# Performance work log

Measured on AMD Instinct MI355X. Metric: run time of the kernel, lower is better.

Reference implementation:

```python
import jax, jax.numpy as jnp
import numpy as np

COLB = 16            # COL_BLOCK_WIDTH
IN_W = 1024          # input_width; zero_inputs=0 so input_locations = arange(IN_W)
OUT_W = 512          # output_width
DEPTH = 8            # network_depth
IN_L = 4             # butterfly_in_depth
OUT_L = 4            # butterfly_out_depth
ACT = 8              # activations_per_block
BLOCKS = 64          # blocks_per_layer -> num_inputs = 1024 per module
CURV = 1.0
GROW = BLOCKS * ACT  # 512 new rows per module
TOTAL = IN_W + DEPTH * GROW  # 5120
BATCH = 4096


def setup_inputs() -> dict:
    key = jax.random.key(0)
    k1, k2, k3 = jax.random.split(key, 3)
    input_data = jax.random.normal(k1, (IN_W, BATCH), dtype=jnp.float32)
    scales = jnp.full((IN_W,), 0.05, dtype=jnp.float32)
    # angles uniform in (-pi, pi), shape [depth, in_layers+out_layers, num_inputs/2]
    angles = (jax.random.uniform(k2, (DEPTH, IN_L + OUT_L, BLOCKS * COLB // 2)) * 2.0 - 1.0) * np.pi
    angles = angles.astype(jnp.float32)
    biases = jax.random.normal(k3, (DEPTH, GROW), dtype=jnp.float32) * 0.05
    # per-module indices_in = randperm(total_width_so_far)[:num_inputs]
    rng = np.random.RandomState(0)
    tw = IN_W
    idxs = []
    for _ in range(DEPTH):
        idxs.append(rng.permutation(tw)[: BLOCKS * COLB].astype(np.int32))
        tw += GROW
    indices_in = jnp.asarray(np.stack(idxs))  # [depth, 1024]
    return {"input_data": input_data, "scales": scales, "angles": angles,
            "biases": biases, "indices_in": indices_in}


def _rotate(x, ang, stride):
    # x: [W, B]; pair row i (with (i//stride)%2==0) with row i+stride inside 16-blocks
    W, B = x.shape
    xr = x.reshape(W // (2 * stride), 2, stride, B)
    a = ang.reshape(W // (2 * stride), stride)[:, :, None]
    c, s = jnp.cos(a), jnp.sin(a)
    lo, hi = xr[:, 0], xr[:, 1]              # [W/2s, s, B]
    nlo = c * lo + s * hi
    nhi = -s * lo + c * hi
    return jnp.stack([nlo, nhi], axis=1).reshape(W, B)


def _butterfly_module(data, ang, bias, idx, idx_out):
    W = BLOCKS * COLB
    x = data[idx]                             # gather [1024, B]
    for l in range(IN_L):
        x = _rotate(x, ang[l], 2 ** (l % 4))
    xb = x.reshape(BLOCKS, COLB, -1)
    pre = xb[:, :ACT, :] + bias.reshape(BLOCKS, ACT)[:, :, None]
    # curvature (smoothed-ReLU) activation
    act = 0.5 * (pre + jnp.sqrt(pre * pre + CURV * CURV))
    xb = xb.at[:, :ACT, :].set(act)
    x = xb.reshape(W, -1)
    for l in range(OUT_L):
        x = _rotate(x, ang[IN_L + l], 2 ** ((IN_L + l) % 4))
    data = data.at[idx].set(x)                # scatter working set back
    data = data.at[idx_out: idx_out + GROW].set(act.reshape(GROW, -1))
    return data


def reference(input_data, scales, angles, biases, indices_in):
    B = input_data.shape[1]
    data = jnp.zeros((TOTAL, B), dtype=input_data.dtype)
    data = data.at[:IN_W].set(scales[:, None] * input_data)
    for i in range(DEPTH):
        data = _butterfly_module(data, angles[i], biases[i], indices_in[i], IN_W + GROW * i)
    return data[TOTAL - OUT_W:]
```

## Files before the change

kernel.cpp:

```cpp
#include <hip/hip_runtime.h>
#include <math.h>

#define N_INW     1024
#define N_DEPTH   8
#define N_GROW    512
#define N_BATCH   4096
#define N_THREADS 128
#define N_LAYERS  64
#define SLAB_B    19584

typedef __attribute__((ext_vector_type(2))) float    F2;
typedef __attribute__((ext_vector_type(2))) _Float16 h2;

__global__ void precompute_kernel(const float* __restrict__ angles,
                                  const int*   __restrict__ indices,
                                  _Float16* __restrict__ csh,
                                  int*   __restrict__ addrs) {
    int i = blockIdx.x * blockDim.x + threadIdx.x;
    if (i < N_LAYERS * 512) {
        int g = i >> 9, p = i & 511, blk = p >> 3, j = p & 7;
        float a = angles[i];
        _Float16* base = csh + g * 1024 + blk * 16;
        base[j]     = (_Float16)cosf(a);
        base[8 + j] = (_Float16)sinf(a);
    }
    if (i < N_DEPTH * N_INW) {
        int v = indices[i];
        addrs[i] = (v + (v >> 4)) << 2;
    }
}

#define ADDR(r) ((((r) + ((r) >> 4))) << 2)

#define LDH(A)    __builtin_bit_cast(h2, *(const unsigned*)(L + (A)))
#define STH(A, V) do { *(unsigned*)(L + (A)) =                                 \
                       __builtin_bit_cast(unsigned, (V)); } while (0)

#define PKU(x, y) __builtin_bit_cast(unsigned int,                             \
                      __builtin_amdgcn_cvt_pkrtz((x), (y)))

#define BCL(U) ({ h2 _t = __builtin_bit_cast(h2, (unsigned)(U));               \
                  h2 _r; _r.x = _t.x; _r.y = _t.x; _r; })
#define BCH(U) ({ h2 _t = __builtin_bit_cast(h2, (unsigned)(U));               \
                  h2 _r; _r.x = _t.y; _r.y = _t.y; _r; })

#define ROTPH(LO, HI, CC, SS) do { h2 _l = LO, _h = HI, _c = CC, _s = SS;      \
    LO = _c * _l + _s * _h; HI = _c * _h - _s * _l; } while (0)

#define DECL_SET(P)                                                            \
    uint4 P##c0, P##s0, P##c1, P##s1, P##c2, P##s2, P##c3, P##s3,              \
          P##c4, P##s4, P##c5, P##s5, P##c6, P##s6, P##c7, P##s7;              \
    int4  P##i0, P##i1, P##i2, P##i3;                                          \
    float4 P##bA, P##bB;

#define SYN1(P, K, ANB) do {                                                   \
    const float4* _p = (const float4*)((ANB) + (K)*512 + (blk << 3));          \
    float4 _u = _p[0], _v = _p[1];                                             \
    float _c0,_c1,_c2,_c3,_c4,_c5,_c6,_c7,_t0,_t1,_t2,_t3,_t4,_t5,_t6,_t7;     \
    __sincosf(_u.x,&_t0,&_c0); __sincosf(_u.y,&_t1,&_c1);                      \
    __sincosf(_u.z,&_t2,&_c2); __sincosf(_u.w,&_t3,&_c3);                      \
    __sincosf(_v.x,&_t4,&_c4); __sincosf(_v.y,&_t5,&_c5);                      \
    __sincosf(_v.z,&_t6,&_c6); __sincosf(_v.w,&_t7,&_c7);                      \
    P##c##K = make_uint4(PKU(_c0,_c1),PKU(_c2,_c3),PKU(_c4,_c5),PKU(_c6,_c7)); \
    P##s##K = make_uint4(PKU(_t0,_t1),PKU(_t2,_t3),PKU(_t4,_t5),PKU(_t6,_t7)); \
  } while (0)

#define LOADCS1(P, K, CSN, ANB) do { if (USE_TABLE) {                          \
    const char* _b = (CSN) + (blk << 5) + (K)*2048;                            \
    P##c##K = *(const uint4*)(_b); P##s##K = *(const uint4*)(_b + 16);         \
  } else { SYN1(P, K, ANB); } } while (0)

#define LOADCS8(P, CSN, ANB) do {                                              \
    LOADCS1(P,0,CSN,ANB); LOADCS1(P,1,CSN,ANB); LOADCS1(P,2,CSN,ANB);          \
    LOADCS1(P,3,CSN,ANB); LOADCS1(P,4,CSN,ANB); LOADCS1(P,5,CSN,ANB);          \
    LOADCS1(P,6,CSN,ANB); LOADCS1(P,7,CSN,ANB); } while (0)
#define LOADCS4(P, CSN, ANB) do {                                              \
    LOADCS1(P,0,CSN,ANB); LOADCS1(P,1,CSN,ANB); LOADCS1(P,2,CSN,ANB);          \
    LOADCS1(P,3,CSN,ANB); } while (0)

#define TR(v) (((v) + ((v) >> 4)) << 2)
#define LOAD_AB(P, ATN, INB, BIN) do { if (USE_TABLE) {                        \
    const int4* _ip = (const int4*)((ATN) + (blk << 4));                       \
    P##i0=_ip[0]; P##i1=_ip[1]; P##i2=_ip[2]; P##i3=_ip[3];                    \
  } else {                                                                     \
    const int4* _ip = (const int4*)((INB) + (blk << 4));                       \
    int4 _v0=_ip[0], _v1=_ip[1], _v2=_ip[2], _v3=_ip[3];                       \
    P##i0.x=TR(_v0.x); P##i0.y=TR(_v0.y); P##i0.z=TR(_v0.z); P##i0.w=TR(_v0.w);\
    P##i1.x=TR(_v1.x); P##i1.y=TR(_v1.y); P##i1.z=TR(_v1.z); P##i1.w=TR(_v1.w);\
    P##i2.x=TR(_v2.x); P##i2.y=TR(_v2.y); P##i2.z=TR(_v2.z); P##i2.w=TR(_v2.w);\
    P##i3.x=TR(_v3.x); P##i3.y=TR(_v3.y); P##i3.z=TR(_v3.z); P##i3.w=TR(_v3.w);\
  }                                                                            \
  const float4* _bp = (const float4*)((BIN) + (blk << 3));                     \
  P##bA = _bp[0]; P##bB = _bp[1]; } while (0)

#define HROTS1(C,S) do {                                                       \
    ROTPH(x0,x1,  BCL(C.x),BCL(S.x)); ROTPH(x2,x3,  BCH(C.x),BCH(S.x));        \
    ROTPH(x4,x5,  BCL(C.y),BCL(S.y)); ROTPH(x6,x7,  BCH(C.y),BCH(S.y));        \
    ROTPH(x8,x9,  BCL(C.z),BCL(S.z)); ROTPH(x10,x11,BCH(C.z),BCH(S.z));        \
    ROTPH(x12,x13,BCL(C.w),BCL(S.w)); ROTPH(x14,x15,BCH(C.w),BCH(S.w));        \
  } while (0)
#define HROTS2(C,S) do {                                                       \
    ROTPH(x0,x2,  BCL(C.x),BCL(S.x)); ROTPH(x1,x3,  BCH(C.x),BCH(S.x));        \
    ROTPH(x4,x6,  BCL(C.y),BCL(S.y)); ROTPH(x5,x7,  BCH(C.y),BCH(S.y));        \
    ROTPH(x8,x10, BCL(C.z),BCL(S.z)); ROTPH(x9,x11, BCH(C.z),BCH(S.z));        \
    ROTPH(x12,x14,BCL(C.w),BCL(S.w)); ROTPH(x13,x15,BCH(C.w),BCH(S.w));        \
  } while (0)
#define HROTS4(C,S) do {                                                       \
    ROTPH(x0,x4,  BCL(C.x),BCL(S.x)); ROTPH(x1,x5,  BCH(C.x),BCH(S.x));        \
    ROTPH(x2,x6,  BCL(C.y),BCL(S.y)); ROTPH(x3,x7,  BCH(C.y),BCH(S.y));        \
    ROTPH(x8,x12, BCL(C.z),BCL(S.z)); ROTPH(x9,x13, BCH(C.z),BCH(S.z));        \
    ROTPH(x10,x14,BCL(C.w),BCL(S.w)); ROTPH(x11,x15,BCH(C.w),BCH(S.w));        \
  } while (0)
#define HROTS8(C,S) do {                                                       \
    ROTPH(x0,x8,  BCL(C.x),BCL(S.x)); ROTPH(x1,x9,  BCH(C.x),BCH(S.x));        \
    ROTPH(x2,x10, BCL(C.y),BCL(S.y)); ROTPH(x3,x11, BCH(C.y),BCH(S.y));        \
    ROTPH(x4,x12, BCL(C.z),BCL(S.z)); ROTPH(x5,x13, BCH(C.z),BCH(S.z));        \
    ROTPH(x6,x14, BCL(C.w),BCL(S.w)); ROTPH(x7,x15, BCH(C.w),BCH(S.w));        \
  } while (0)

#define HROT(P, K, M) M(P##c##K, P##s##K)

#define ACTH(X, BF) do {                                                       \
    float _lo = (float)(X).x + (BF), _hi = (float)(X).y + (BF);                \
    _lo = 0.5f * (_lo + __builtin_amdgcn_sqrtf(_lo * _lo + 1.0f));             \
    _hi = 0.5f * (_hi + __builtin_amdgcn_sqrtf(_hi * _hi + 1.0f));             \
    X = __builtin_bit_cast(h2, PKU(_lo, _hi)); } while (0)

#define FENCE() __builtin_amdgcn_sched_barrier(0)

#define PROC_MOD(P, N, CSN, ANN, ATN, INB, BIN, M, FULL) do {                  \
  const int a0=P##i0.x, a1=P##i0.y, a2=P##i0.z, a3=P##i0.w,                    \
            a4=P##i1.x, a5=P##i1.y, a6=P##i1.z, a7=P##i1.w,                    \
            a8=P##i2.x, a9=P##i2.y, a10=P##i2.z, a11=P##i2.w,                  \
            a12=P##i3.x, a13=P##i3.y, a14=P##i3.z, a15=P##i3.w;                \
  h2 x0=LDH(a0), x1=LDH(a1), x2=LDH(a2), x3=LDH(a3),                           \
     x4=LDH(a4), x5=LDH(a5), x6=LDH(a6), x7=LDH(a7),                           \
     x8=LDH(a8), x9=LDH(a9), x10=LDH(a10), x11=LDH(a11),                       \
     x12=LDH(a12), x13=LDH(a13), x14=LDH(a14), x15=LDH(a15);                   \
  if (FULL) { LOADCS8(N, CSN, ANN); } else { LOADCS4(N, CSN, ANN); }           \
  FENCE();                                                                     \
  HROT(P,0,HROTS1); HROT(P,1,HROTS2); HROT(P,2,HROTS4); HROT(P,3,HROTS8);      \
  ACTH(x0,P##bA.x); ACTH(x1,P##bA.y); ACTH(x2,P##bA.z); ACTH(x3,P##bA.w);      \
  ACTH(x4,P##bB.x); ACTH(x5,P##bB.y); ACTH(x6,P##bB.z); ACTH(x7,P##bB.w);      \
  const int _ab = ADDR(N_INW + (M)*N_GROW + (blk << 3));                       \
  STH(_ab+ 0,x0); STH(_ab+ 4,x1); STH(_ab+ 8,x2); STH(_ab+12,x3);              \
  STH(_ab+16,x4); STH(_ab+20,x5); STH(_ab+24,x6); STH(_ab+28,x7);              \
  LOAD_AB(N, ATN, INB, BIN);                                                   \
  FENCE();                                                                     \
  HROT(P,4,HROTS1); HROT(P,5,HROTS2); HROT(P,6,HROTS4); HROT(P,7,HROTS8);      \
  STH(a0,x0);  STH(a1,x1);  STH(a2,x2);  STH(a3,x3);                           \
  STH(a4,x4);  STH(a5,x5);  STH(a6,x6);  STH(a7,x7);                           \
  STH(a8,x8);  STH(a9,x9);  STH(a10,x10); STH(a11,x11);                        \
  STH(a12,x12); STH(a13,x13); STH(a14,x14); STH(a15,x15);                      \
} while (0)

template <bool USE_TABLE>
__global__ __launch_bounds__(N_THREADS, 2)
void butterfly_fused_kernel(const float* __restrict__ input,
                            const float* __restrict__ scales,
                            const float* __restrict__ biases,
                            const int*   __restrict__ indices,
                            const char*  __restrict__ cs_tab,
                            const int*   __restrict__ addr_tab,
                            const float* __restrict__ angles,
                            float* __restrict__ out) {
    extern __shared__ float ldsbuf[];
    const int t   = threadIdx.x;
    const int blk = t & 63;
    const int cp  = t >> 6;
    char* L = (char*)ldsbuf + cp * SLAB_B;
    const int b   = blockIdx.x;
    const int cg  = ((((b & 7) * 128) + (b >> 3)) << 2) + (cp << 1);

    DECL_SET(A) DECL_SET(B)

    LOADCS8(A, cs_tab, angles);
    LOAD_AB(A, addr_tab, indices, biases);

#pragma unroll
    for (int k = 0; k < 16; ++k) {
        const int r = (k << 6) + blk;
        F2 v = *(const F2*)(input + (size_t)r * N_BATCH + cg);
        STH(ADDR(r), __builtin_bit_cast(h2, PKU(scales[r] * v.x, scales[r] * v.y)));
    }

    const char*  csn = cs_tab + 16384;
    const float* ann = angles + 4096;
    const int*   atn = addr_tab + N_INW;
    const int*   inb = indices + N_INW;
    const float* bin = biases + N_GROW;

#pragma unroll 1
    for (int tt = 0; tt < 3; ++tt) {
        const int m = 2 * tt;
        PROC_MOD(A, B, csn, ann, atn, inb, bin, m, 1);
        csn += 16384; ann += 4096; atn += N_INW; inb += N_INW; bin += N_GROW;
        PROC_MOD(B, A, csn, ann, atn, inb, bin, m + 1, 1);
        csn += 16384; ann += 4096; atn += N_INW; inb += N_INW; bin += N_GROW;
    }
    PROC_MOD(A, B, csn, ann, atn, inb, bin, 6, 0);

    {
        h2 x0=LDH(Bi0.x), x1=LDH(Bi0.y), x2=LDH(Bi0.z), x3=LDH(Bi0.w),
           x4=LDH(Bi1.x), x5=LDH(Bi1.y), x6=LDH(Bi1.z), x7=LDH(Bi1.w),
           x8=LDH(Bi2.x), x9=LDH(Bi2.y), x10=LDH(Bi2.z), x11=LDH(Bi2.w),
           x12=LDH(Bi3.x), x13=LDH(Bi3.y), x14=LDH(Bi3.z), x15=LDH(Bi3.w);
        FENCE();
        HROT(B,0,HROTS1); HROT(B,1,HROTS2); HROT(B,2,HROTS4); HROT(B,3,HROTS8);
        ACTH(x0,BbA.x); ACTH(x1,BbA.y); ACTH(x2,BbA.z); ACTH(x3,BbA.w);
        ACTH(x4,BbB.x); ACTH(x5,BbB.y); ACTH(x6,BbB.z); ACTH(x7,BbB.w);
#define OUTW(J, X) do { F2 _o; _o.x = (float)(X).x; _o.y = (float)(X).y;       \
        *(F2*)(out + (size_t)((blk<<3)+(J))*N_BATCH + cg) = _o; } while (0)
        OUTW(0,x0); OUTW(1,x1); OUTW(2,x2); OUTW(3,x3);
        OUTW(4,x4); OUTW(5,x5); OUTW(6,x6); OUTW(7,x7);
#undef OUTW
    }
}

extern "C" void kernel_launch(void* const* d_in, const int* in_sizes, int n_in,
                              void* d_out, int out_size, void* d_ws, size_t ws_size,
                              hipStream_t stream) {
    const float* input   = (const float*)d_in[0];
    const float* scales  = (const float*)d_in[1];
    const float* angles  = (const float*)d_in[2];
    const float* biases  = (const float*)d_in[3];
    const int*   indices = (const int*)d_in[4];
    float* out = (float*)d_out;

    const size_t cs_bytes  = (size_t)N_LAYERS * 2048;
    const size_t adr_bytes = (size_t)N_DEPTH * N_INW * sizeof(int);
    const size_t lds_bytes = (size_t)2 * SLAB_B;
    const int grid = N_BATCH / 4;

    if (ws_size >= cs_bytes + adr_bytes) {
        _Float16* csh = (_Float16*)d_ws;
        int* addrs = (int*)((char*)d_ws + cs_bytes);
        precompute_kernel<<<(N_LAYERS * 512 + 255) / 256, 256, 0, stream>>>(
            angles, indices, csh, addrs);
        butterfly_fused_kernel<true><<<grid, N_THREADS, lds_bytes, stream>>>(
            input, scales, biases, indices, (const char*)csh, addrs, angles, out);
    } else {
        butterfly_fused_kernel<false><<<grid, N_THREADS, lds_bytes, stream>>>(
            input, scales, biases, indices, nullptr, nullptr, angles, out);
    }
}
```

Baseline: 98.33 us.

## Process one batch column per thread with row-packed half2 butterflies

Each thread now handles one batch column instead of two. Two rows of the same column are packed into a half2, so the stride-1 rotation uses a lane swap and the larger strides pair whole half2 registers. LDS per slab drops from about 19.5KB to 9KB and holds plain 2-byte rows with no padding. The grid doubles and launch bounds rise to 4 blocks per SM to raise occupancy. The cost is 16-bit LDS gathers and scatters, which double the LDS operation count, uncoalesced single-float global accesses, and the loss of the A/B double-buffered prefetch of the next module's parameters.

```diff
diff --git a/kernel.cpp b/kernel.cpp
--- a/kernel.cpp
+++ b/kernel.cpp
@@ -7,9 +7,8 @@
 #define N_BATCH   4096
 #define N_THREADS 128
 #define N_LAYERS  64
-#define SLAB_B    19584
-
-typedef __attribute__((ext_vector_type(2))) float    F2;
+#define SLAB_B    9216
+
 typedef __attribute__((ext_vector_type(2))) _Float16 h2;
 
 __global__ void precompute_kernel(const float* __restrict__ angles,
@@ -24,138 +23,94 @@
         base[j]     = (_Float16)cosf(a);
         base[8 + j] = (_Float16)sinf(a);
     }
-    if (i < N_DEPTH * N_INW) {
-        int v = indices[i];
-        addrs[i] = (v + (v >> 4)) << 2;
-    }
+    if (i < N_DEPTH * N_INW) addrs[i] = indices[i] << 1;
 }
 
-#define ADDR(r) ((((r) + ((r) >> 4))) << 2)
-
-#define LDH(A)    __builtin_bit_cast(h2, *(const unsigned*)(L + (A)))
-#define STH(A, V) do { *(unsigned*)(L + (A)) =                                 \
-                       __builtin_bit_cast(unsigned, (V)); } while (0)
-
-#define PKU(x, y) __builtin_bit_cast(unsigned int,                             \
-                      __builtin_amdgcn_cvt_pkrtz((x), (y)))
-
-#define BCL(U) ({ h2 _t = __builtin_bit_cast(h2, (unsigned)(U));               \
-                  h2 _r; _r.x = _t.x; _r.y = _t.x; _r; })
-#define BCH(U) ({ h2 _t = __builtin_bit_cast(h2, (unsigned)(U));               \
-                  h2 _r; _r.x = _t.y; _r.y = _t.y; _r; })
-
-#define ROTPH(LO, HI, CC, SS) do { h2 _l = LO, _h = HI, _c = CC, _s = SS;      \
-    LO = _c * _l + _s * _h; HI = _c * _h - _s * _l; } while (0)
-
-#define DECL_SET(P)                                                            \
-    uint4 P##c0, P##s0, P##c1, P##s1, P##c2, P##s2, P##c3, P##s3,              \
-          P##c4, P##s4, P##c5, P##s5, P##c6, P##s6, P##c7, P##s7;              \
-    int4  P##i0, P##i1, P##i2, P##i3;                                          \
-    float4 P##bA, P##bB;
-
-#define SYN1(P, K, ANB) do {                                                   \
-    const float4* _p = (const float4*)((ANB) + (K)*512 + (blk << 3));          \
+#define H(U)   __builtin_bit_cast(h2, (unsigned)(U))
+#define PKU(x, y) __builtin_bit_cast(unsigned, __builtin_amdgcn_cvt_pkrtz((x), (y)))
+#define BCL(U) ({ h2 _t = H(U); h2 _r; _r.x = _t.x; _r.y = _t.x; _r; })
+#define BCH(U) ({ h2 _t = H(U); h2 _r; _r.x = _t.y; _r.y = _t.y; _r; })
+#define BCLN(U) H(__builtin_bit_cast(unsigned, BCL(U)) ^ 0x80000000u)
+#define BCHN(U) H(__builtin_bit_cast(unsigned, BCH(U)) ^ 0x80000000u)
+
+#define R1(Y, CC, SN) do { unsigned _u = __builtin_bit_cast(unsigned, Y);      \
+    h2 _sw = H((_u << 16) | (_u >> 16));                                       \
+    Y = (CC) * (Y) + (SN) * _sw; } while (0)
+#define RS1(C, S) do {                                                         \
+    R1(y0, BCL(C.x), BCLN(S.x)); R1(y1, BCH(C.x), BCHN(S.x));                  \
+    R1(y2, BCL(C.y), BCLN(S.y)); R1(y3, BCH(C.y), BCHN(S.y));                  \
+    R1(y4, BCL(C.z), BCLN(S.z)); R1(y5, BCH(C.z), BCHN(S.z));                  \
+    R1(y6, BCL(C.w), BCLN(S.w)); R1(y7, BCH(C.w), BCHN(S.w)); } while (0)
+#define RP(YA, YB, CH, SH) do { h2 _a = YA, _b = YB, _c = CH, _s = SH;         \
+    YA = _c * _a + _s * _b; YB = _c * _b - _s * _a; } while (0)
+#define RS2(C, S) do { RP(y0,y1,H(C.x),H(S.x)); RP(y2,y3,H(C.y),H(S.y));       \
+    RP(y4,y5,H(C.z),H(S.z)); RP(y6,y7,H(C.w),H(S.w)); } while (0)
+#define RS4(C, S) do { RP(y0,y2,H(C.x),H(S.x)); RP(y1,y3,H(C.y),H(S.y));       \
+    RP(y4,y6,H(C.z),H(S.z)); RP(y5,y7,H(C.w),H(S.w)); } while (0)
+#define RS8(C, S) do { RP(y0,y4,H(C.x),H(S.x)); RP(y1,y5,H(C.y),H(S.y));       \
+    RP(y2,y6,H(C.z),H(S.z)); RP(y3,y7,H(C.w),H(S.w)); } while (0)
+
+#define LDCS(CK, SK, G) do { if (USE_TABLE) {                                  \
+    const char* _b = csl + (G) * 2048;                                         \
+    CK = *(const uint4*)(_b); SK = *(const uint4*)(_b + 16);                   \
+  } else {                                                                     \
+    const float4* _p = (const float4*)(anl + (G) * 512);                       \
     float4 _u = _p[0], _v = _p[1];                                             \
     float _c0,_c1,_c2,_c3,_c4,_c5,_c6,_c7,_t0,_t1,_t2,_t3,_t4,_t5,_t6,_t7;     \
     __sincosf(_u.x,&_t0,&_c0); __sincosf(_u.y,&_t1,&_c1);                      \
     __sincosf(_u.z,&_t2,&_c2); __sincosf(_u.w,&_t3,&_c3);                      \
     __sincosf(_v.x,&_t4,&_c4); __sincosf(_v.y,&_t5,&_c5);                      \
     __sincosf(_v.z,&_t6,&_c6); __sincosf(_v.w,&_t7,&_c7);                      \
-    P##c##K = make_uint4(PKU(_c0,_c1),PKU(_c2,_c3),PKU(_c4,_c5),PKU(_c6,_c7)); \
-    P##s##K = make_uint4(PKU(_t0,_t1),PKU(_t2,_t3),PKU(_t4,_t5),PKU(_t6,_t7)); \
-  } while (0)
-
-#define LOADCS1(P, K, CSN, ANB) do { if (USE_TABLE) {                          \
-    const char* _b = (CSN) + (blk << 5) + (K)*2048;                            \
-    P##c##K = *(const uint4*)(_b); P##s##K = *(const uint4*)(_b + 16);         \
-  } else { SYN1(P, K, ANB); } } while (0)
-
-#define LOADCS8(P, CSN, ANB) do {                                              \
-    LOADCS1(P,0,CSN,ANB); LOADCS1(P,1,CSN,ANB); LOADCS1(P,2,CSN,ANB);          \
-    LOADCS1(P,3,CSN,ANB); LOADCS1(P,4,CSN,ANB); LOADCS1(P,5,CSN,ANB);          \
-    LOADCS1(P,6,CSN,ANB); LOADCS1(P,7,CSN,ANB); } while (0)
-#define LOADCS4(P, CSN, ANB) do {                                              \
-    LOADCS1(P,0,CSN,ANB); LOADCS1(P,1,CSN,ANB); LOADCS1(P,2,CSN,ANB);          \
-    LOADCS1(P,3,CSN,ANB); } while (0)
-
-#define TR(v) (((v) + ((v) >> 4)) << 2)
-#define LOAD_AB(P, ATN, INB, BIN) do { if (USE_TABLE) {                        \
-    const int4* _ip = (const int4*)((ATN) + (blk << 4));                       \
-    P##i0=_ip[0]; P##i1=_ip[1]; P##i2=_ip[2]; P##i3=_ip[3];                    \
+    CK = make_uint4(PKU(_c0,_c1),PKU(_c2,_c3),PKU(_c4,_c5),PKU(_c6,_c7));      \
+    SK = make_uint4(PKU(_t0,_t1),PKU(_t2,_t3),PKU(_t4,_t5),PKU(_t6,_t7));      \
+  } } while (0)
+
+#define LDADDR() do { if (USE_TABLE) {                                         \
+    const int4* _ip = (const int4*)(atl);                                      \
+    i0 = _ip[0]; i1 = _ip[1]; i2 = _ip[2]; i3 = _ip[3];                        \
   } else {                                                                     \
-    const int4* _ip = (const int4*)((INB) + (blk << 4));                       \
-    int4 _v0=_ip[0], _v1=_ip[1], _v2=_ip[2], _v3=_ip[3];                       \
-    P##i0.x=TR(_v0.x); P##i0.y=TR(_v0.y); P##i0.z=TR(_v0.z); P##i0.w=TR(_v0.w);\
-    P##i1.x=TR(_v1.x); P##i1.y=TR(_v1.y); P##i1.z=TR(_v1.z); P##i1.w=TR(_v1.w);\
-    P##i2.x=TR(_v2.x); P##i2.y=TR(_v2.y); P##i2.z=TR(_v2.z); P##i2.w=TR(_v2.w);\
-    P##i3.x=TR(_v3.x); P##i3.y=TR(_v3.y); P##i3.z=TR(_v3.z); P##i3.w=TR(_v3.w);\
-  }                                                                            \
-  const float4* _bp = (const float4*)((BIN) + (blk << 3));                     \
-  P##bA = _bp[0]; P##bB = _bp[1]; } while (0)
-
-#define HROTS1(C,S) do {                                                       \
-    ROTPH(x0,x1,  BCL(C.x),BCL(S.x)); ROTPH(x2,x3,  BCH(C.x),BCH(S.x));        \
-    ROTPH(x4,x5,  BCL(C.y),BCL(S.y)); ROTPH(x6,x7,  BCH(C.y),BCH(S.y));        \
-    ROTPH(x8,x9,  BCL(C.z),BCL(S.z)); ROTPH(x10,x11,BCH(C.z),BCH(S.z));        \
-    ROTPH(x12,x13,BCL(C.w),BCL(S.w)); ROTPH(x14,x15,BCH(C.w),BCH(S.w));        \
-  } while (0)
-#define HROTS2(C,S) do {                                                       \
-    ROTPH(x0,x2,  BCL(C.x),BCL(S.x)); ROTPH(x1,x3,  BCH(C.x),BCH(S.x));        \
-    ROTPH(x4,x6,  BCL(C.y),BCL(S.y)); ROTPH(x5,x7,  BCH(C.y),BCH(S.y));        \
-    ROTPH(x8,x10, BCL(C.z),BCL(S.z)); ROTPH(x9,x11, BCH(C.z),BCH(S.z));        \
-    ROTPH(x12,x14,BCL(C.w),BCL(S.w)); ROTPH(x13,x15,BCH(C.w),BCH(S.w));        \
-  } while (0)
-#define HROTS4(C,S) do {                                                       \
-    ROTPH(x0,x4,  BCL(C.x),BCL(S.x)); ROTPH(x1,x5,  BCH(C.x),BCH(S.x));        \
-    ROTPH(x2,x6,  BCL(C.y),BCL(S.y)); ROTPH(x3,x7,  BCH(C.y),BCH(S.y));        \
-    ROTPH(x8,x12, BCL(C.z),BCL(S.z)); ROTPH(x9,x13, BCH(C.z),BCH(S.z));        \
-    ROTPH(x10,x14,BCL(C.w),BCL(S.w)); ROTPH(x11,x15,BCH(C.w),BCH(S.w));        \
-  } while (0)
-#define HROTS8(C,S) do {                                                       \
-    ROTPH(x0,x8,  BCL(C.x),BCL(S.x)); ROTPH(x1,x9,  BCH(C.x),BCH(S.x));        \
-    ROTPH(x2,x10, BCL(C.y),BCL(S.y)); ROTPH(x3,x11, BCH(C.y),BCH(S.y));        \
-    ROTPH(x4,x12, BCL(C.z),BCL(S.z)); ROTPH(x5,x13, BCH(C.z),BCH(S.z));        \
-    ROTPH(x6,x14, BCL(C.w),BCL(S.w)); ROTPH(x7,x15, BCH(C.w),BCH(S.w));        \
-  } while (0)
-
-#define HROT(P, K, M) M(P##c##K, P##s##K)
-
-#define ACTH(X, BF) do {                                                       \
-    float _lo = (float)(X).x + (BF), _hi = (float)(X).y + (BF);                \
+    const int4* _ip = (const int4*)(inl);                                      \
+    int4 _a = _ip[0], _b = _ip[1], _c = _ip[2], _d = _ip[3];                   \
+    i0.x=_a.x<<1; i0.y=_a.y<<1; i0.z=_a.z<<1; i0.w=_a.w<<1;                    \
+    i1.x=_b.x<<1; i1.y=_b.y<<1; i1.z=_b.z<<1; i1.w=_b.w<<1;                    \
+    i2.x=_c.x<<1; i2.y=_c.y<<1; i2.z=_c.z<<1; i2.w=_c.w<<1;                    \
+    i3.x=_d.x<<1; i3.y=_d.y<<1; i3.z=_d.z<<1; i3.w=_d.w<<1;                    \
+  } } while (0)
+
+#define LDBIAS() do { const float4* _bp = (const float4*)(bil);                \
+    float4 _a = _bp[0], _b = _bp[1];                                           \
+    bb0 = H(PKU(_a.x,_a.y)); bb1 = H(PKU(_a.z,_a.w));                          \
+    bb2 = H(PKU(_b.x,_b.y)); bb3 = H(PKU(_b.z,_b.w)); } while (0)
+
+#define GPAIR(Y, A0, A1) do {                                                  \
+    unsigned _lo = *(const unsigned short*)(L + (A0));                         \
+    unsigned _hi = *(const unsigned short*)(L + (A1));                         \
+    Y = H(_lo | (_hi << 16)); } while (0)
+#define SPAIR(Y, A0, A1) do { unsigned _w = __builtin_bit_cast(unsigned, Y);   \
+    *(unsigned short*)(L + (A0)) = (unsigned short)_w;                         \
+    *(unsigned short*)(L + (A1)) = (unsigned short)(_w >> 16); } while (0)
+#define GATHER() do {                                                          \
+    GPAIR(y0, i0.x, i0.y); GPAIR(y1, i0.z, i0.w);                              \
+    GPAIR(y2, i1.x, i1.y); GPAIR(y3, i1.z, i1.w);                              \
+    GPAIR(y4, i2.x, i2.y); GPAIR(y5, i2.z, i2.w);                              \
+    GPAIR(y6, i3.x, i3.y); GPAIR(y7, i3.z, i3.w); } while (0)
+#define SCATTER() do {                                                         \
+    SPAIR(y0, i0.x, i0.y); SPAIR(y1, i0.z, i0.w);                              \
+    SPAIR(y2, i1.x, i1.y); SPAIR(y3, i1.z, i1.w);                              \
+    SPAIR(y4, i2.x, i2.y); SPAIR(y5, i2.z, i2.w);                              \
+    SPAIR(y6, i3.x, i3.y); SPAIR(y7, i3.z, i3.w); } while (0)
+
+#define ACT(Y, BB) do {                                                        \
+    float _lo = (float)(Y).x + (float)(BB).x;                                  \
+    float _hi = (float)(Y).y + (float)(BB).y;                                  \
     _lo = 0.5f * (_lo + __builtin_amdgcn_sqrtf(_lo * _lo + 1.0f));             \
     _hi = 0.5f * (_hi + __builtin_amdgcn_sqrtf(_hi * _hi + 1.0f));             \
-    X = __builtin_bit_cast(h2, PKU(_lo, _hi)); } while (0)
+    Y = H(PKU(_lo, _hi)); } while (0)
 
 #define FENCE() __builtin_amdgcn_sched_barrier(0)
 
-#define PROC_MOD(P, N, CSN, ANN, ATN, INB, BIN, M, FULL) do {                  \
-  const int a0=P##i0.x, a1=P##i0.y, a2=P##i0.z, a3=P##i0.w,                    \
-            a4=P##i1.x, a5=P##i1.y, a6=P##i1.z, a7=P##i1.w,                    \
-            a8=P##i2.x, a9=P##i2.y, a10=P##i2.z, a11=P##i2.w,                  \
-            a12=P##i3.x, a13=P##i3.y, a14=P##i3.z, a15=P##i3.w;                \
-  h2 x0=LDH(a0), x1=LDH(a1), x2=LDH(a2), x3=LDH(a3),                           \
-     x4=LDH(a4), x5=LDH(a5), x6=LDH(a6), x7=LDH(a7),                           \
-     x8=LDH(a8), x9=LDH(a9), x10=LDH(a10), x11=LDH(a11),                       \
-     x12=LDH(a12), x13=LDH(a13), x14=LDH(a14), x15=LDH(a15);                   \
-  if (FULL) { LOADCS8(N, CSN, ANN); } else { LOADCS4(N, CSN, ANN); }           \
-  FENCE();                                                                     \
-  HROT(P,0,HROTS1); HROT(P,1,HROTS2); HROT(P,2,HROTS4); HROT(P,3,HROTS8);      \
-  ACTH(x0,P##bA.x); ACTH(x1,P##bA.y); ACTH(x2,P##bA.z); ACTH(x3,P##bA.w);      \
-  ACTH(x4,P##bB.x); ACTH(x5,P##bB.y); ACTH(x6,P##bB.z); ACTH(x7,P##bB.w);      \
-  const int _ab = ADDR(N_INW + (M)*N_GROW + (blk << 3));                       \
-  STH(_ab+ 0,x0); STH(_ab+ 4,x1); STH(_ab+ 8,x2); STH(_ab+12,x3);              \
-  STH(_ab+16,x4); STH(_ab+20,x5); STH(_ab+24,x6); STH(_ab+28,x7);              \
-  LOAD_AB(N, ATN, INB, BIN);                                                   \
-  FENCE();                                                                     \
-  HROT(P,4,HROTS1); HROT(P,5,HROTS2); HROT(P,6,HROTS4); HROT(P,7,HROTS8);      \
-  STH(a0,x0);  STH(a1,x1);  STH(a2,x2);  STH(a3,x3);                           \
-  STH(a4,x4);  STH(a5,x5);  STH(a6,x6);  STH(a7,x7);                           \
-  STH(a8,x8);  STH(a9,x9);  STH(a10,x10); STH(a11,x11);                        \
-  STH(a12,x12); STH(a13,x13); STH(a14,x14); STH(a15,x15);                      \
-} while (0)
-
 template <bool USE_TABLE>
-__global__ __launch_bounds__(N_THREADS, 2)
+__global__ __launch_bounds__(N_THREADS, 4)
 void butterfly_fused_kernel(const float* __restrict__ input,
                             const float* __restrict__ scales,
                             const float* __restrict__ biases,
@@ -164,56 +119,70 @@
                             const int*   __restrict__ addr_tab,
                             const float* __restrict__ angles,
                             float* __restrict__ out) {
-    extern __shared__ float ldsbuf[];
+    extern __shared__ char ldsbuf[];
     const int t   = threadIdx.x;
     const int blk = t & 63;
     const int cp  = t >> 6;
-    char* L = (char*)ldsbuf + cp * SLAB_B;
+    char* L = ldsbuf + cp * SLAB_B;
     const int b   = blockIdx.x;
-    const int cg  = ((((b & 7) * 128) + (b >> 3)) << 2) + (cp << 1);
-
-    DECL_SET(A) DECL_SET(B)
-
-    LOADCS8(A, cs_tab, angles);
-    LOAD_AB(A, addr_tab, indices, biases);
+    const int cg  = (((b & 7) * 256) + (b >> 3)) * 2 + cp;
+
+    const char*  csl = cs_tab + (blk << 5);
+    const float* anl = angles + (blk << 3);
+    const int*   atl = addr_tab + (blk << 4);
+    const int*   inl = indices + (blk << 4);
+    const float* bil = biases + (blk << 3);
+
+    uint4 cI0,sI0,cI1,sI1,cI2,sI2,cI3,sI3;
+    uint4 cO0,sO0,cO1,sO1,cO2,sO2,cO3,sO3;
+    int4  i0, i1, i2, i3;
+    h2    bb0, bb1, bb2, bb3;
+    h2    y0, y1, y2, y3, y4, y5, y6, y7;
+
+    LDCS(cI0,sI0,0); LDCS(cI1,sI1,1); LDCS(cI2,sI2,2); LDCS(cI3,sI3,3);
 
 #pragma unroll
     for (int k = 0; k < 16; ++k) {
         const int r = (k << 6) + blk;
-        F2 v = *(const F2*)(input + (size_t)r * N_BATCH + cg);
-        STH(ADDR(r), __builtin_bit_cast(h2, PKU(scales[r] * v.x, scales[r] * v.y)));
-    }
-
-    const char*  csn = cs_tab + 16384;
-    const float* ann = angles + 4096;
-    const int*   atn = addr_tab + N_INW;
-    const int*   inb = indices + N_INW;
-    const float* bin = biases + N_GROW;
+        float v = scales[r] * input[(size_t)r * N_BATCH + cg];
+        *(unsigned short*)(L + (r << 1)) =
+            __builtin_bit_cast(unsigned short, (_Float16)v);
+    }
 
 #pragma unroll 1
-    for (int tt = 0; tt < 3; ++tt) {
-        const int m = 2 * tt;
-        PROC_MOD(A, B, csn, ann, atn, inb, bin, m, 1);
-        csn += 16384; ann += 4096; atn += N_INW; inb += N_INW; bin += N_GROW;
-        PROC_MOD(B, A, csn, ann, atn, inb, bin, m + 1, 1);
-        csn += 16384; ann += 4096; atn += N_INW; inb += N_INW; bin += N_GROW;
-    }
-    PROC_MOD(A, B, csn, ann, atn, inb, bin, 6, 0);
+    for (int m = 0; m < 7; ++m) {
+        LDADDR(); LDBIAS();
+        GATHER();
+        LDCS(cO0,sO0,4); LDCS(cO1,sO1,5); LDCS(cO2,sO2,6); LDCS(cO3,sO3,7);
+        FENCE();
+        RS1(cI0,sI0); RS2(cI1,sI1); RS4(cI2,sI2); RS8(cI3,sI3);
+        ACT(y0,bb0); ACT(y1,bb1); ACT(y2,bb2); ACT(y3,bb3);
+        { unsigned* ap = (unsigned*)(L + 2048 + m * 1024 + (blk << 4));
+          ap[0] = __builtin_bit_cast(unsigned, y0);
+          ap[1] = __builtin_bit_cast(unsigned, y1);
+          ap[2] = __builtin_bit_cast(unsigned, y2);
+          ap[3] = __builtin_bit_cast(unsigned, y3); }
+        LDCS(cI0,sI0,8); LDCS(cI1,sI1,9); LDCS(cI2,sI2,10); LDCS(cI3,sI3,11);
+        FENCE();
+        RS1(cO0,sO0); RS2(cO1,sO1); RS4(cO2,sO2); RS8(cO3,sO3);
+        SCATTER();
+        csl += 16384; anl += 4096; atl += N_INW; inl += N_INW; bil += N_GROW;
+    }
 
     {
-        h2 x0=LDH(Bi0.x), x1=LDH(Bi0.y), x2=LDH(Bi0.z), x3=LDH(Bi0.w),
-           x4=LDH(Bi1.x), x5=LDH(Bi1.y), x6=LDH(Bi1.z), x7=LDH(Bi1.w),
-           x8=LDH(Bi2.x), x9=LDH(Bi2.y), x10=LDH(Bi2.z), x11=LDH(Bi2.w),
-           x12=LDH(Bi3.x), x13=LDH(Bi3.y), x14=LDH(Bi3.z), x15=LDH(Bi3.w);
+        LDADDR(); LDBIAS();
+        GATHER();
         FENCE();
-        HROT(B,0,HROTS1); HROT(B,1,HROTS2); HROT(B,2,HROTS4); HROT(B,3,HROTS8);
-        ACTH(x0,BbA.x); ACTH(x1,BbA.y); ACTH(x2,BbA.z); ACTH(x3,BbA.w);
-        ACTH(x4,BbB.x); ACTH(x5,BbB.y); ACTH(x6,BbB.z); ACTH(x7,BbB.w);
-#define OUTW(J, X) do { F2 _o; _o.x = (float)(X).x; _o.y = (float)(X).y;       \
-        *(F2*)(out + (size_t)((blk<<3)+(J))*N_BATCH + cg) = _o; } while (0)
-        OUTW(0,x0); OUTW(1,x1); OUTW(2,x2); OUTW(3,x3);
-        OUTW(4,x4); OUTW(5,x5); OUTW(6,x6); OUTW(7,x7);
-#undef OUTW
+        RS1(cI0,sI0); RS2(cI1,sI1); RS4(cI2,sI2); RS8(cI3,sI3);
+        ACT(y0,bb0); ACT(y1,bb1); ACT(y2,bb2); ACT(y3,bb3);
+        out[(size_t)((blk<<3)+0)*N_BATCH + cg] = (float)y0.x;
+        out[(size_t)((blk<<3)+1)*N_BATCH + cg] = (float)y0.y;
+        out[(size_t)((blk<<3)+2)*N_BATCH + cg] = (float)y1.x;
+        out[(size_t)((blk<<3)+3)*N_BATCH + cg] = (float)y1.y;
+        out[(size_t)((blk<<3)+4)*N_BATCH + cg] = (float)y2.x;
+        out[(size_t)((blk<<3)+5)*N_BATCH + cg] = (float)y2.y;
+        out[(size_t)((blk<<3)+6)*N_BATCH + cg] = (float)y3.x;
+        out[(size_t)((blk<<3)+7)*N_BATCH + cg] = (float)y3.y;
     }
 }
 
@@ -230,7 +199,7 @@
     const size_t cs_bytes  = (size_t)N_LAYERS * 2048;
     const size_t adr_bytes = (size_t)N_DEPTH * N_INW * sizeof(int);
     const size_t lds_bytes = (size_t)2 * SLAB_B;
-    const int grid = N_BATCH / 4;
+    const int grid = N_BATCH / 2;
 
     if (ws_size >= cs_bytes + adr_bytes) {
         _Float16* csh = (_Float16*)d_ws;
```

Measured after the change: 113.6 us. 1.16x slower.
